# Performance work log

Hardware: AMD Instinct MI355X
Metric: run time of the kernel (lower is better)

## Reference

```python
import jax, jax.numpy as jnp
import numpy as np

B, A, C, M = 4, 120000, 80, 32
ALPHA, GAMMA, EPS = 0.75, 2.0, 1e-4
STD = np.array([0.1, 0.1, 0.2, 0.2, 0.1, 0.1, 0.2, 0.2], dtype=np.float32)


def _make_boxes(key, shape, img=1024.0):
    k1, k2, k3, k4 = jax.random.split(key, 4)
    cx = jax.random.uniform(k1, shape) * img
    cy = jax.random.uniform(k2, shape) * img
    w = jax.random.uniform(k3, shape) * 224.0 + 32.0
    h = jax.random.uniform(k4, shape) * 224.0 + 32.0
    return jnp.stack([cx - 0.5 * w, cy - 0.5 * h, cx + 0.5 * w, cy + 0.5 * h], axis=-1)


def setup_inputs() -> dict:
    key = jax.random.key(0)
    kc, kr, ka, kh, kf, kl, ki = jax.random.split(key, 7)
    classifications = jax.random.uniform(kc, (B, A, C), dtype=jnp.float32)
    regressions = jax.random.normal(kr, (B, A, 8), dtype=jnp.float32)
    anchors = _make_boxes(ka, (1, A))  # [1,A,4]
    head = _make_boxes(kh, (B, M))     # [B,M,4]
    full = _make_boxes(kf, (B, M))     # [B,M,4]
    labels = jax.random.randint(kl, (B, M, 1), 0, C).astype(jnp.float32)
    ignore = jax.random.randint(ki, (B, M, 1), 0, 2).astype(jnp.float32)
    annotations = jnp.concatenate([head, full, labels, ignore], axis=-1)  # [B,M,10]
    return {"classifications": classifications, "regressions": regressions,
            "anchors": anchors, "annotations": annotations}


def _calc_iou(a, b):
    # a: [A,4], b: [B,M,4] -> [B,A,M]
    area_b = (b[..., 2] - b[..., 0]) * (b[..., 3] - b[..., 1])  # [B,M]
    a = a[None, :, None, :]
    bb = b[:, None, :, :]
    iw = jnp.clip(jnp.minimum(a[..., 2], bb[..., 2]) - jnp.maximum(a[..., 0], bb[..., 0]), 0.0)
    ih = jnp.clip(jnp.minimum(a[..., 3], bb[..., 3]) - jnp.maximum(a[..., 1], bb[..., 1]), 0.0)
    area_a = ((a[..., 2] - a[..., 0]) * (a[..., 3] - a[..., 1]))  # [1,A,1]
    inter = iw * ih
    ua = jnp.clip(area_a + area_b[:, None, :] - inter, 1e-8)
    return inter / ua


def reference(classifications, regressions, anchors, annotations):
    anchor = anchors[0]                       # [A,4]
    aw = anchor[:, 2] - anchor[:, 0]
    ah = anchor[:, 3] - anchor[:, 1]
    acx = anchor[:, 0] + 0.5 * aw
    acy = anchor[:, 1] + 0.5 * ah

    ann = annotations[..., :-1]               # [B,M,9]
    full_box = ann[..., 4:8]

    iou = _calc_iou(anchor, full_box)         # [B,A,M]
    iou_max = jnp.max(iou, axis=-1)           # [B,A]
    iou_arg = jnp.argmax(iou, axis=-1)        # [B,A]

    pos = iou_max >= 0.5                      # [B,A]
    neg = iou_max < 0.4
    num_pos = jnp.sum(pos, axis=1).astype(jnp.float32)  # [B]

    assigned = jnp.take_along_axis(ann, iou_arg[..., None], axis=1)  # [B,A,9]
    assigned_cls = assigned[..., 8].astype(jnp.int32)                # [B,A]

    one_hot = jax.nn.one_hot(assigned_cls, classifications.shape[-1], dtype=jnp.float32)
    targets = jnp.where(pos[..., None], one_hot,
                        jnp.where(neg[..., None], 0.0, -1.0))        # [B,A,C]

    p = jnp.clip(classifications, EPS, 1.0 - EPS)
    alpha_f = jnp.where(targets == 1.0, ALPHA, 1.0 - ALPHA)
    focal_w = alpha_f * jnp.where(targets == 1.0, 1.0 - p, p) ** GAMMA
    bce = -(targets * jnp.log(p) + (1.0 - targets) * jnp.log(1.0 - p))
    cls_loss = jnp.where(targets != -1.0, focal_w * bce, 0.0)
    cls_losses = jnp.sum(cls_loss, axis=(1, 2)) / jnp.clip(num_pos, 1.0)  # [B]

    gw_h = assigned[..., 2] - assigned[..., 0]
    gh_h = assigned[..., 3] - assigned[..., 1]
    gcx_h = assigned[..., 0] + 0.5 * gw_h
    gcy_h = assigned[..., 1] + 0.5 * gh_h
    gw_f = assigned[..., 6] - assigned[..., 4]
    gh_f = assigned[..., 7] - assigned[..., 5]
    gcx_f = assigned[..., 4] + 0.5 * gw_f
    gcy_f = assigned[..., 5] + 0.5 * gh_f
    gw_h = jnp.clip(gw_h, 1.0); gh_h = jnp.clip(gh_h, 1.0)
    gw_f = jnp.clip(gw_f, 1.0); gh_f = jnp.clip(gh_f, 1.0)

    t = jnp.stack([
        (gcx_f - acx) / aw, (gcy_f - acy) / ah,
        jnp.log(gw_f / aw), jnp.log(gh_f / ah),
        (gcx_h - acx) / aw * 4.0, (gcy_h - acy) / ah * 4.0,
        jnp.log(gw_h / aw * 4.0), jnp.log(gh_h / ah * 4.0),
    ], axis=-1) / jnp.asarray(STD)            # [B,A,8]

    diff = jnp.abs(t - regressions)
    # only_full=True: weights zero out cols 4:8
    diff = diff * jnp.asarray([1., 1., 1., 1., 0., 0., 0., 0.], dtype=jnp.float32)
    rl = jnp.where(diff <= 1.0 / 9.0, 0.5 * 9.0 * diff * diff, diff - 0.5 / 9.0)
    rl4 = rl[..., 0:4] * pos[..., None]       # [B,A,4], only positive anchors
    reg_losses = jnp.where(num_pos > 0,
                           jnp.sum(rl4, axis=(1, 2)) / (jnp.clip(num_pos, 1.0) * 4.0),
                           0.0)               # mean over positive rows x 4 cols

    return (jnp.mean(cls_losses, keepdims=True), jnp.mean(reg_losses, keepdims=True))
```

## Files before the change

kernel.cpp:

```cpp
#include <hip/hip_runtime.h>

#define NB 4
#define NA 120000
#define NC 80
#define NM 32

#define EPS_   1e-4f
#define LN2_   0.69314718055994531f

constexpr int BLOCK = 256;
constexpr int APB   = 64;
constexpr int U     = 5;
constexpr int BINS  = 64;

__device__ __forceinline__ float wave_reduce_f(float v) {
    #pragma unroll
    for (int off = 32; off > 0; off >>= 1) v += __shfl_down(v, off, 64);
    return v;
}
__device__ __forceinline__ double wave_reduce_d(double v) {
    #pragma unroll
    for (int off = 32; off > 0; off >>= 1) v += __shfl_down(v, off, 64);
    return v;
}

__device__ __forceinline__ float flog2(float x) { return __builtin_amdgcn_logf(x); }

__global__ __launch_bounds__(BLOCK)
void focal_fused(const float* __restrict__ cls,
                 const float* __restrict__ reg,
                 const float* __restrict__ anchors,
                 const float* __restrict__ ann,
                 double* __restrict__ acc)
{
    __shared__ float s_ann[NM * 10];
    __shared__ float s_coef[APB];
    __shared__ float s_red[4];
    __shared__ float s_rp[2];

    const int b   = blockIdx.y;
    const int a0  = blockIdx.x * APB;
    const int tid = threadIdx.x;

    const float* annB = ann + b * NM * 10;
    if (tid < NM * 10 - BLOCK) s_ann[BLOCK + tid] = annB[BLOCK + tid];
    s_ann[tid] = annB[tid];
    __syncthreads();

    float regLoss = 0.0f;
    float posCnt  = 0.0f;
    float clsCorr = 0.0f;

    if (tid < APB) {
        const int a = a0 + tid;
        const float4 an = ((const float4*)anchors)[a];
        const float ax1 = an.x, ay1 = an.y, ax2 = an.z, ay2 = an.w;
        const float aw  = ax2 - ax1, ah = ay2 - ay1;
        const float acx = ax1 + 0.5f * aw, acy = ay1 + 0.5f * ah;
        const float areaA = aw * ah;

        float best = -1.0f;
        int   arg  = 0;
        #pragma unroll
        for (int m = 0; m < NM; ++m) {
            const float bx1 = s_ann[m * 10 + 4];
            const float by1 = s_ann[m * 10 + 5];
            const float bx2 = s_ann[m * 10 + 6];
            const float by2 = s_ann[m * 10 + 7];
            float iw = fminf(ax2, bx2) - fmaxf(ax1, bx1); iw = fmaxf(iw, 0.0f);
            float ih = fminf(ay2, by2) - fmaxf(ay1, by1); ih = fmaxf(ih, 0.0f);
            const float inter = iw * ih;
            const float areaB = (bx2 - bx1) * (by2 - by1);
            const float ua    = fmaxf(areaA + areaB - inter, 1e-8f);
            const float iou   = inter / ua;
            if (iou > best) { best = iou; arg = m; }
        }

        const bool pos = best >= 0.5f;
        const bool neg = best < 0.4f;
        s_coef[tid] = (pos || neg) ? (-0.25f * LN2_) : 0.0f;

        if (pos) {
            posCnt = 1.0f;
            const int c = (int)s_ann[arg * 10 + 8];
            const float xc = cls[((size_t)b * NA + a) * NC + c];
            const float p  = fminf(fmaxf(xc, EPS_), 1.0f - EPS_);
            const float q  = 1.0f - p;
            const float posT = 0.75f * q * q * (-LN2_ * flog2(p));
            const float negT = 0.25f * p * p * (-LN2_ * flog2(q));
            clsCorr = posT - negT;

            const float fx1 = s_ann[arg * 10 + 4];
            const float fy1 = s_ann[arg * 10 + 5];
            const float fx2 = s_ann[arg * 10 + 6];
            const float fy2 = s_ann[arg * 10 + 7];
            float gw = fx2 - fx1, gh = fy2 - fy1;
            const float gcx = fx1 + 0.5f * gw, gcy = fy1 + 0.5f * gh;
            gw = fmaxf(gw, 1.0f); gh = fmaxf(gh, 1.0f);
            const float t0 = ((gcx - acx) / aw) * 10.0f;
            const float t1 = ((gcy - acy) / ah) * 10.0f;
            const float t2 = (LN2_ * flog2(gw / aw)) * 5.0f;
            const float t3 = (LN2_ * flog2(gh / ah)) * 5.0f;
            const float4 r4 = ((const float4*)reg)[(size_t)(b * NA + a) * 2];
            const float d0 = fabsf(t0 - r4.x);
            const float d1 = fabsf(t1 - r4.y);
            const float d2 = fabsf(t2 - r4.z);
            const float d3 = fabsf(t3 - r4.w);
            const float beta = 1.0f / 9.0f;
            #define SL1(d) ((d) <= beta ? 4.5f * (d) * (d) : (d) - 0.5f / 9.0f)
            regLoss = SL1(d0) + SL1(d1) + SL1(d2) + SL1(d3);
            #undef SL1
        }
    }
    __syncthreads();

    const float4* base4 = (const float4*)(cls + (size_t)b * NA * NC) + (size_t)a0 * (NC / 4);

    float4 x[U];
    #pragma unroll
    for (int j = 0; j < U; ++j)
        x[j] = base4[j * BLOCK + tid];

    float clsSum = clsCorr;
    #pragma unroll
    for (int j = 0; j < U; ++j) {
        const int idx = j * BLOCK + tid;
        const float C = s_coef[idx / (NC / 4)];
        const float4 x4 = x[j];

        float p0 = fminf(fmaxf(x4.x, EPS_), 1.0f - EPS_);
        float p1 = fminf(fmaxf(x4.y, EPS_), 1.0f - EPS_);
        float p2 = fminf(fmaxf(x4.z, EPS_), 1.0f - EPS_);
        float p3 = fminf(fmaxf(x4.w, EPS_), 1.0f - EPS_);

        float t0 = p0 * p0 * flog2(1.0f - p0);
        float t1 = p1 * p1 * flog2(1.0f - p1);
        float t2 = p2 * p2 * flog2(1.0f - p2);
        float t3 = p3 * p3 * flog2(1.0f - p3);

        clsSum = fmaf((t0 + t1) + (t2 + t3), C, clsSum);
    }

    const int wave = tid >> 6, lane = tid & 63;
    float rc = wave_reduce_f(clsSum);
    if (lane == 0) s_red[wave] = rc;
    if (wave == 0) {
        float rr = wave_reduce_f(regLoss);
        float rp = wave_reduce_f(posCnt);
        if (lane == 0) { s_rp[0] = rr; s_rp[1] = rp; }
    }
    __syncthreads();
    if (tid == 0) {
        const float c = (s_red[0] + s_red[1]) + (s_red[2] + s_red[3]);
        const int bin = blockIdx.x & (BINS - 1);
        atomicAdd(&acc[(b * 3 + 0) * BINS + bin], (double)c);
        atomicAdd(&acc[(b * 3 + 1) * BINS + bin], (double)s_rp[0]);
        atomicAdd(&acc[(b * 3 + 2) * BINS + bin], (double)s_rp[1]);
    }
}

__global__ void focal_finalize(const double* __restrict__ acc, float* __restrict__ out) {
    __shared__ double g[NB * 3];
    const int tid  = threadIdx.x;
    const int wave = tid >> 6, lane = tid & 63;
    double v = acc[wave * BINS + lane];
    v = wave_reduce_d(v);
    if (lane == 0) g[wave] = v;
    __syncthreads();
    if (tid == 0) {
        double clsTot = 0.0, regTot = 0.0;
        #pragma unroll
        for (int b = 0; b < NB; ++b) {
            const double np  = g[b * 3 + 2];
            const double npc = np < 1.0 ? 1.0 : np;
            clsTot += g[b * 3 + 0] / npc;
            regTot += (np > 0.0) ? g[b * 3 + 1] / (npc * 4.0) : 0.0;
        }
        out[0] = (float)(clsTot / NB);
        out[1] = (float)(regTot / NB);
    }
}

extern "C" void kernel_launch(void* const* d_in, const int* in_sizes, int n_in,
                              void* d_out, int out_size, void* d_ws, size_t ws_size,
                              hipStream_t stream) {
    const float* cls     = (const float*)d_in[0];
    const float* reg     = (const float*)d_in[1];
    const float* anchors = (const float*)d_in[2];
    const float* ann     = (const float*)d_in[3];
    float* out = (float*)d_out;
    double* acc = (double*)d_ws;

    hipMemsetAsync(acc, 0, NB * 3 * BINS * sizeof(double), stream);

    dim3 grid(NA / APB, NB);
    focal_fused<<<grid, BLOCK, 0, stream>>>(cls, reg, anchors, ann, acc);
    focal_finalize<<<1, NB * 3 * BINS, 0, stream>>>(acc, out);
}
```

Before: 235.9 us.

## Split fused kernel into anchor-metadata kernel and classification streaming kernel

Moves the per-anchor IoU matching, positive-anchor correction and regression loss into a separate kernel where every thread handles one anchor, instead of only a quarter of the threads working while the rest idle. The per-anchor coefficient goes to a global buffer that a second, purely streaming kernel reads while it reduces the classification tensor. This removes the serial IoU phase that stalled the bandwidth-bound stream in each block. The cost is an extra kernel launch and a small global write and read of the coefficients.

```diff
diff --git a/kernel.cpp b/kernel.cpp
--- a/kernel.cpp
+++ b/kernel.cpp
@@ -8,10 +8,11 @@
 #define EPS_   1e-4f
 #define LN2_   0.69314718055994531f
 
-constexpr int BLOCK = 256;
-constexpr int APB   = 64;
-constexpr int U     = 5;
-constexpr int BINS  = 64;
+constexpr int MBLOCK = 192;
+constexpr int SBLOCK = 256;
+constexpr int APB    = 64;
+constexpr int U      = 5;
+constexpr int BINS   = 64;
 
 __device__ __forceinline__ float wave_reduce_f(float v) {
     #pragma unroll
@@ -26,33 +27,28 @@
 
 __device__ __forceinline__ float flog2(float x) { return __builtin_amdgcn_logf(x); }
 
-__global__ __launch_bounds__(BLOCK)
-void focal_fused(const float* __restrict__ cls,
-                 const float* __restrict__ reg,
-                 const float* __restrict__ anchors,
-                 const float* __restrict__ ann,
-                 double* __restrict__ acc)
+__global__ __launch_bounds__(MBLOCK)
+void focal_meta(const float* __restrict__ cls,
+                const float* __restrict__ reg,
+                const float* __restrict__ anchors,
+                const float* __restrict__ ann,
+                float* __restrict__ coef,
+                double* __restrict__ acc)
 {
     __shared__ float s_ann[NM * 10];
-    __shared__ float s_coef[APB];
-    __shared__ float s_red[4];
-    __shared__ float s_rp[2];
+    __shared__ float s_red[3][3];
 
     const int b   = blockIdx.y;
-    const int a0  = blockIdx.x * APB;
     const int tid = threadIdx.x;
+    const int a   = blockIdx.x * MBLOCK + tid;
 
     const float* annB = ann + b * NM * 10;
-    if (tid < NM * 10 - BLOCK) s_ann[BLOCK + tid] = annB[BLOCK + tid];
     s_ann[tid] = annB[tid];
-    __syncthreads();
-
-    float regLoss = 0.0f;
-    float posCnt  = 0.0f;
-    float clsCorr = 0.0f;
-
-    if (tid < APB) {
-        const int a = a0 + tid;
+    if (tid < NM * 10 - MBLOCK) s_ann[MBLOCK + tid] = annB[MBLOCK + tid];
+    __syncthreads();
+
+    float regLoss = 0.0f, posCnt = 0.0f, clsCorr = 0.0f;
+    {
         const float4 an = ((const float4*)anchors)[a];
         const float ax1 = an.x, ay1 = an.y, ax2 = an.z, ay2 = an.w;
         const float aw  = ax2 - ax1, ah = ay2 - ay1;
@@ -78,7 +74,7 @@
 
         const bool pos = best >= 0.5f;
         const bool neg = best < 0.4f;
-        s_coef[tid] = (pos || neg) ? (-0.25f * LN2_) : 0.0f;
+        coef[(size_t)b * NA + a] = (pos || neg) ? (-0.25f * LN2_) : 0.0f;
 
         if (pos) {
             posCnt = 1.0f;
@@ -112,6 +108,37 @@
             #undef SL1
         }
     }
+
+    const int wave = tid >> 6, lane = tid & 63;
+    float rc = wave_reduce_f(clsCorr);
+    float rr = wave_reduce_f(regLoss);
+    float rp = wave_reduce_f(posCnt);
+    if (lane == 0) { s_red[0][wave] = rc; s_red[1][wave] = rr; s_red[2][wave] = rp; }
+    __syncthreads();
+    if (tid == 0) {
+        const float c = s_red[0][0] + s_red[0][1] + s_red[0][2];
+        const float r = s_red[1][0] + s_red[1][1] + s_red[1][2];
+        const float p = s_red[2][0] + s_red[2][1] + s_red[2][2];
+        const int bin = blockIdx.x & (BINS - 1);
+        atomicAdd(&acc[(b * 3 + 0) * BINS + bin], (double)c);
+        atomicAdd(&acc[(b * 3 + 1) * BINS + bin], (double)r);
+        atomicAdd(&acc[(b * 3 + 2) * BINS + bin], (double)p);
+    }
+}
+
+__global__ __launch_bounds__(SBLOCK)
+void focal_stream(const float* __restrict__ cls,
+                  const float* __restrict__ coef,
+                  double* __restrict__ acc)
+{
+    __shared__ float s_coef[APB];
+    __shared__ float s_red[4];
+
+    const int b   = blockIdx.y;
+    const int a0  = blockIdx.x * APB;
+    const int tid = threadIdx.x;
+
+    if (tid < APB) s_coef[tid] = coef[(size_t)b * NA + a0 + tid];
     __syncthreads();
 
     const float4* base4 = (const float4*)(cls + (size_t)b * NA * NC) + (size_t)a0 * (NC / 4);
@@ -119,12 +146,12 @@
     float4 x[U];
     #pragma unroll
     for (int j = 0; j < U; ++j)
-        x[j] = base4[j * BLOCK + tid];
-
-    float clsSum = clsCorr;
+        x[j] = base4[j * SBLOCK + tid];
+
+    float clsSum = 0.0f;
     #pragma unroll
     for (int j = 0; j < U; ++j) {
-        const int idx = j * BLOCK + tid;
+        const int idx = j * SBLOCK + tid;
         const float C = s_coef[idx / (NC / 4)];
         const float4 x4 = x[j];
 
@@ -144,18 +171,11 @@
     const int wave = tid >> 6, lane = tid & 63;
     float rc = wave_reduce_f(clsSum);
     if (lane == 0) s_red[wave] = rc;
-    if (wave == 0) {
-        float rr = wave_reduce_f(regLoss);
-        float rp = wave_reduce_f(posCnt);
-        if (lane == 0) { s_rp[0] = rr; s_rp[1] = rp; }
-    }
     __syncthreads();
     if (tid == 0) {
         const float c = (s_red[0] + s_red[1]) + (s_red[2] + s_red[3]);
         const int bin = blockIdx.x & (BINS - 1);
         atomicAdd(&acc[(b * 3 + 0) * BINS + bin], (double)c);
-        atomicAdd(&acc[(b * 3 + 1) * BINS + bin], (double)s_rp[0]);
-        atomicAdd(&acc[(b * 3 + 2) * BINS + bin], (double)s_rp[1]);
     }
 }
 
@@ -188,12 +208,17 @@
     const float* reg     = (const float*)d_in[1];
     const float* anchors = (const float*)d_in[2];
     const float* ann     = (const float*)d_in[3];
-    float* out = (float*)d_out;
+    float* out  = (float*)d_out;
     double* acc = (double*)d_ws;
+    float* coef = (float*)((char*)d_ws + 8192);
 
     hipMemsetAsync(acc, 0, NB * 3 * BINS * sizeof(double), stream);
 
-    dim3 grid(NA / APB, NB);
-    focal_fused<<<grid, BLOCK, 0, stream>>>(cls, reg, anchors, ann, acc);
+    dim3 gridA(NA / MBLOCK, NB);
+    focal_meta<<<gridA, MBLOCK, 0, stream>>>(cls, reg, anchors, ann, coef, acc);
+
+    dim3 gridB(NA / APB, NB);
+    focal_stream<<<gridB, SBLOCK, 0, stream>>>(cls, coef, acc);
+
     focal_finalize<<<1, NB * 3 * BINS, 0, stream>>>(acc, out);
 }
```

Measured after the change: 244.7 us. 1.04x slower.

## Convert focal loss kernel to persistent grid with per-wave anchor chunks

Applied to the files above, without the earlier changes.

Replaces the one-block-per-64-anchors grid with a persistent grid of 512 blocks per batch image that loop over 64-anchor chunks. Each wave handles 16 anchors, and the IoU argmax is split across 4 lanes per anchor and merged with xor shuffles. The per-anchor coefficient is broadcast through wave shuffles instead of shared memory, which removes the intermediate __syncthreads and the idle three-quarters of the block during the IoU phase. Class loads are issued before the IoU math to overlap memory latency. The cost is a tie-break rule in the shuffle merge that must match the original first-max argmax order, and a loop over fewer, longer-lived blocks.

```diff
diff --git a/kernel.cpp b/kernel.cpp
--- a/kernel.cpp
+++ b/kernel.cpp
@@ -8,10 +8,13 @@
 #define EPS_   1e-4f
 #define LN2_   0.69314718055994531f
 
-constexpr int BLOCK = 256;
-constexpr int APB   = 64;
-constexpr int U     = 5;
-constexpr int BINS  = 64;
+constexpr int BLOCK  = 256;
+constexpr int WPB    = 4;
+constexpr int APW    = 16;
+constexpr int APC    = WPB * APW;
+constexpr int NCHUNK = NA / APC;
+constexpr int BPB    = 512;
+constexpr int BINS   = 64;
 
 __device__ __forceinline__ float wave_reduce_f(float v) {
     #pragma unroll
@@ -26,43 +29,55 @@
 
 __device__ __forceinline__ float flog2(float x) { return __builtin_amdgcn_logf(x); }
 
-__global__ __launch_bounds__(BLOCK)
-void focal_fused(const float* __restrict__ cls,
-                 const float* __restrict__ reg,
-                 const float* __restrict__ anchors,
-                 const float* __restrict__ ann,
-                 double* __restrict__ acc)
+__global__ __launch_bounds__(BLOCK, 8)
+void focal_persist(const float* __restrict__ cls,
+                   const float* __restrict__ reg,
+                   const float* __restrict__ anchors,
+                   const float* __restrict__ ann,
+                   double* __restrict__ acc)
 {
     __shared__ float s_ann[NM * 10];
-    __shared__ float s_coef[APB];
-    __shared__ float s_red[4];
-    __shared__ float s_rp[2];
-
-    const int b   = blockIdx.y;
-    const int a0  = blockIdx.x * APB;
-    const int tid = threadIdx.x;
-
-    const float* annB = ann + b * NM * 10;
-    if (tid < NM * 10 - BLOCK) s_ann[BLOCK + tid] = annB[BLOCK + tid];
-    s_ann[tid] = annB[tid];
+    __shared__ float s_red[3][WPB];
+
+    const int b    = blockIdx.x >> 9;
+    const int blk  = blockIdx.x & (BPB - 1);
+    const int tid  = threadIdx.x;
+    const int wave = tid >> 6;
+    const int lane = tid & 63;
+    const int aloc = lane >> 2;
+    const int part = lane & 3;
+
+    s_ann[tid < NM * 10 ? tid : 0] = ann[b * NM * 10 + (tid < NM * 10 ? tid : 0)];
+    if (tid < NM * 10 - BLOCK) s_ann[BLOCK + tid] = ann[b * NM * 10 + BLOCK + tid];
     __syncthreads();
 
-    float regLoss = 0.0f;
-    float posCnt  = 0.0f;
-    float clsCorr = 0.0f;
-
-    if (tid < APB) {
-        const int a = a0 + tid;
-        const float4 an = ((const float4*)anchors)[a];
+    float clsSum = 0.0f, regLoss = 0.0f, posCnt = 0.0f;
+
+    const float4* anchors4 = (const float4*)anchors;
+    const float4* cls4b    = (const float4*)cls + (size_t)b * NA * (NC / 4);
+
+    for (int c = blk; c < NCHUNK; c += BPB) {
+        const int aw0 = c * APC + wave * APW;
+        const int a   = aw0 + aloc;
+
+        const float4 an = anchors4[a];
+        const float4* w4 = cls4b + (size_t)aw0 * (NC / 4);
+        float4 x0 = w4[lane];
+        float4 x1 = w4[lane + 64];
+        float4 x2 = w4[lane + 128];
+        float4 x3 = w4[lane + 192];
+        float4 x4_ = w4[lane + 256];
+
         const float ax1 = an.x, ay1 = an.y, ax2 = an.z, ay2 = an.w;
-        const float aw  = ax2 - ax1, ah = ay2 - ay1;
-        const float acx = ax1 + 0.5f * aw, acy = ay1 + 0.5f * ah;
-        const float areaA = aw * ah;
+        const float aw_ = ax2 - ax1, ah = ay2 - ay1;
+        const float acx = ax1 + 0.5f * aw_, acy = ay1 + 0.5f * ah;
+        const float areaA = aw_ * ah;
 
         float best = -1.0f;
         int   arg  = 0;
         #pragma unroll
-        for (int m = 0; m < NM; ++m) {
+        for (int i = 0; i < 8; ++i) {
+            const int m = part * 8 + i;
             const float bx1 = s_ann[m * 10 + 4];
             const float by1 = s_ann[m * 10 + 5];
             const float bx2 = s_ann[m * 10 + 6];
@@ -75,20 +90,25 @@
             const float iou   = inter / ua;
             if (iou > best) { best = iou; arg = m; }
         }
+        #pragma unroll
+        for (int d = 1; d <= 2; d <<= 1) {
+            const float ob = __shfl_xor(best, d, 64);
+            const int   oa = __shfl_xor(arg,  d, 64);
+            if (ob > best || (ob == best && oa < arg)) { best = ob; arg = oa; }
+        }
 
         const bool pos = best >= 0.5f;
         const bool neg = best < 0.4f;
-        s_coef[tid] = (pos || neg) ? (-0.25f * LN2_) : 0.0f;
-
-        if (pos) {
-            posCnt = 1.0f;
-            const int c = (int)s_ann[arg * 10 + 8];
-            const float xc = cls[((size_t)b * NA + a) * NC + c];
+        const float coefL = (pos || neg) ? (-0.25f * LN2_) : 0.0f;
+
+        if (pos && part == 0) {
+            posCnt += 1.0f;
+            const int cc = (int)s_ann[arg * 10 + 8];
+            const float xc = cls[((size_t)b * NA + a) * NC + cc];
             const float p  = fminf(fmaxf(xc, EPS_), 1.0f - EPS_);
             const float q  = 1.0f - p;
-            const float posT = 0.75f * q * q * (-LN2_ * flog2(p));
-            const float negT = 0.25f * p * p * (-LN2_ * flog2(q));
-            clsCorr = posT - negT;
+            clsSum += 0.75f * q * q * (-LN2_ * flog2(p))
+                    - 0.25f * p * p * (-LN2_ * flog2(q));
 
             const float fx1 = s_ann[arg * 10 + 4];
             const float fy1 = s_ann[arg * 10 + 5];
@@ -97,10 +117,10 @@
             float gw = fx2 - fx1, gh = fy2 - fy1;
             const float gcx = fx1 + 0.5f * gw, gcy = fy1 + 0.5f * gh;
             gw = fmaxf(gw, 1.0f); gh = fmaxf(gh, 1.0f);
-            const float t0 = ((gcx - acx) / aw) * 10.0f;
-            const float t1 = ((gcy - acy) / ah) * 10.0f;
-            const float t2 = (LN2_ * flog2(gw / aw)) * 5.0f;
-            const float t3 = (LN2_ * flog2(gh / ah)) * 5.0f;
+            const float t0 = ((gcx - acx) / aw_) * 10.0f;
+            const float t1 = ((gcy - acy) / ah)  * 10.0f;
+            const float t2 = (LN2_ * flog2(gw / aw_)) * 5.0f;
+            const float t3 = (LN2_ * flog2(gh / ah))  * 5.0f;
             const float4 r4 = ((const float4*)reg)[(size_t)(b * NA + a) * 2];
             const float d0 = fabsf(t0 - r4.x);
             const float d1 = fabsf(t1 - r4.y);
@@ -108,54 +128,41 @@
             const float d3 = fabsf(t3 - r4.w);
             const float beta = 1.0f / 9.0f;
             #define SL1(d) ((d) <= beta ? 4.5f * (d) * (d) : (d) - 0.5f / 9.0f)
-            regLoss = SL1(d0) + SL1(d1) + SL1(d2) + SL1(d3);
+            regLoss += SL1(d0) + SL1(d1) + SL1(d2) + SL1(d3);
             #undef SL1
         }
+
+        #define TERM(XV, J)                                                      \
+        {                                                                        \
+            const int idx = lane + 64 * (J);                                     \
+            const float C = __shfl(coefL, (idx / (NC / 4)) << 2, 64);            \
+            float p0 = fminf(fmaxf((XV).x, EPS_), 1.0f - EPS_);                  \
+            float p1 = fminf(fmaxf((XV).y, EPS_), 1.0f - EPS_);                  \
+            float p2 = fminf(fmaxf((XV).z, EPS_), 1.0f - EPS_);                  \
+            float p3 = fminf(fmaxf((XV).w, EPS_), 1.0f - EPS_);                  \
+            float t0 = p0 * p0 * flog2(1.0f - p0);                               \
+            float t1 = p1 * p1 * flog2(1.0f - p1);                               \
+            float t2 = p2 * p2 * flog2(1.0f - p2);                               \
+            float t3 = p3 * p3 * flog2(1.0f - p3);                               \
+            clsSum = fmaf((t0 + t1) + (t2 + t3), C, clsSum);                     \
+        }
+        TERM(x0, 0) TERM(x1, 1) TERM(x2, 2) TERM(x3, 3) TERM(x4_, 4)
+        #undef TERM
     }
-    __syncthreads();
-
-    const float4* base4 = (const float4*)(cls + (size_t)b * NA * NC) + (size_t)a0 * (NC / 4);
-
-    float4 x[U];
-    #pragma unroll
-    for (int j = 0; j < U; ++j)
-        x[j] = base4[j * BLOCK + tid];
-
-    float clsSum = clsCorr;
-    #pragma unroll
-    for (int j = 0; j < U; ++j) {
-        const int idx = j * BLOCK + tid;
-        const float C = s_coef[idx / (NC / 4)];
-        const float4 x4 = x[j];
-
-        float p0 = fminf(fmaxf(x4.x, EPS_), 1.0f - EPS_);
-        float p1 = fminf(fmaxf(x4.y, EPS_), 1.0f - EPS_);
-        float p2 = fminf(fmaxf(x4.z, EPS_), 1.0f - EPS_);
-        float p3 = fminf(fmaxf(x4.w, EPS_), 1.0f - EPS_);
-
-        float t0 = p0 * p0 * flog2(1.0f - p0);
-        float t1 = p1 * p1 * flog2(1.0f - p1);
-        float t2 = p2 * p2 * flog2(1.0f - p2);
-        float t3 = p3 * p3 * flog2(1.0f - p3);
-
-        clsSum = fmaf((t0 + t1) + (t2 + t3), C, clsSum);
-    }
-
-    const int wave = tid >> 6, lane = tid & 63;
+
     float rc = wave_reduce_f(clsSum);
-    if (lane == 0) s_red[wave] = rc;
-    if (wave == 0) {
-        float rr = wave_reduce_f(regLoss);
-        float rp = wave_reduce_f(posCnt);
-        if (lane == 0) { s_rp[0] = rr; s_rp[1] = rp; }
-    }
+    float rr = wave_reduce_f(regLoss);
+    float rp = wave_reduce_f(posCnt);
+    if (lane == 0) { s_red[0][wave] = rc; s_red[1][wave] = rr; s_red[2][wave] = rp; }
     __syncthreads();
     if (tid == 0) {
-        const float c = (s_red[0] + s_red[1]) + (s_red[2] + s_red[3]);
+        const float c = (s_red[0][0] + s_red[0][1]) + (s_red[0][2] + s_red[0][3]);
+        const float r = (s_red[1][0] + s_red[1][1]) + (s_red[1][2] + s_red[1][3]);
+        const float p = (s_red[2][0] + s_red[2][1]) + (s_red[2][2] + s_red[2][3]);
         const int bin = blockIdx.x & (BINS - 1);
         atomicAdd(&acc[(b * 3 + 0) * BINS + bin], (double)c);
-        atomicAdd(&acc[(b * 3 + 1) * BINS + bin], (double)s_rp[0]);
-        atomicAdd(&acc[(b * 3 + 2) * BINS + bin], (double)s_rp[1]);
+        atomicAdd(&acc[(b * 3 + 1) * BINS + bin], (double)r);
+        atomicAdd(&acc[(b * 3 + 2) * BINS + bin], (double)p);
     }
 }
 
@@ -188,12 +195,11 @@
     const float* reg     = (const float*)d_in[1];
     const float* anchors = (const float*)d_in[2];
     const float* ann     = (const float*)d_in[3];
-    float* out = (float*)d_out;
+    float* out  = (float*)d_out;
     double* acc = (double*)d_ws;
 
     hipMemsetAsync(acc, 0, NB * 3 * BINS * sizeof(double), stream);
 
-    dim3 grid(NA / APB, NB);
-    focal_fused<<<grid, BLOCK, 0, stream>>>(cls, reg, anchors, ann, acc);
+    focal_persist<<<NB * BPB, BLOCK, 0, stream>>>(cls, reg, anchors, ann, acc);
     focal_finalize<<<1, NB * 3 * BINS, 0, stream>>>(acc, out);
 }
```

New measurement: 264.2 us. 1.12x slower.
